# Performance work log

Hardware: AMD Instinct MI355X
Metric: run time of the kernel (lower is better)

Reference implementation:

```python
import jax, jax.numpy as jnp
import numpy as np

N_NODES = 10000
N_EDGES = 160000
C = 64        # latent channels
H = 512       # MLP hidden width
L = 2         # allegro layers
NB = 8        # bessel basis size
CUT = 2.0     # radial cutoff
AVG = 3.0     # avg_num_neighbors


def setup_inputs() -> dict:
    key = jax.random.key(0)
    ks = jax.random.split(key, 12)
    positions = jax.random.normal(ks[0], (N_NODES, 3), jnp.float32)
    species = jax.random.randint(ks[1], (N_NODES,), 0, 2, jnp.int32)
    senders = jax.random.randint(ks[2], (N_EDGES,), 0, N_NODES, jnp.int32)
    receivers = jax.random.randint(ks[3], (N_EDGES,), 0, N_NODES, jnp.int32)
    w = lambda k, shape, fan: (jax.random.normal(k, shape, jnp.float32) / np.sqrt(fan).astype(np.float32))
    return dict(
        positions=positions,
        W_emb1=w(ks[4], (NB + 4, H), NB + 4),
        W_emb2=w(ks[5], (H, C), H),
        W_v=w(ks[6], (C, C), C),
        W_env=w(ks[7], (L, C, C), C),
        W_lat1=w(ks[8], (L, 3 * C, H), 3 * C),
        W_lat2=w(ks[9], (L, H, C), H),
        W_mix=w(ks[10], (L, C, 2 * C), C),
        W_out=w(ks[11], (C,), C),
        species=species, senders=senders, receivers=receivers,
    )


def reference(positions, W_emb1, W_emb2, W_v, W_env, W_lat1, W_lat2, W_mix, W_out,
              species, senders, receivers):
    node_attrs = jax.nn.one_hot(species, 2, dtype=positions.dtype)   # [N,2]
    r = positions[receivers] - positions[senders]                    # [E,3] edge vectors ('1o')
    d = jnp.sqrt(jnp.sum(r * r, axis=-1))                            # [E]
    dsafe = jnp.maximum(d, 1e-6)
    u = r / dsafe[:, None]                                           # unit vectors = l=1 spherical harmonics

    # radial basis: Bessel functions with smooth polynomial cutoff envelope
    xc = d / CUT
    env = jnp.where(xc < 1.0, (1.0 - xc ** 2) ** 2, 0.0)             # [E]
    nvec = jnp.arange(1, NB + 1, dtype=positions.dtype)
    bessel = jnp.sqrt(2.0 / CUT) * jnp.sin(nvec * jnp.pi * xc[:, None]) / dsafe[:, None]
    rad = bessel * env[:, None]                                      # [E,NB]

    # two-body latent embedding
    feat = jnp.concatenate([rad, node_attrs[senders], node_attrs[receivers]], axis=-1)  # [E,NB+4]
    x = (jax.nn.silu(feat @ W_emb1) @ W_emb2) * env[:, None]         # [E,C]
    # initial equivariant edge features (C channels of 1o)
    V = (x @ W_v)[:, :, None] * u[:, None, :]                        # [E,C,3]

    inv_sqrt2 = 1.0 / jnp.sqrt(2.0)
    for l in range(L):
        # environment density: scatter edge basis to sender nodes, gather back per edge
        w_e = x @ W_env[l]                                           # [E,C]
        rho1 = jax.ops.segment_sum(w_e[:, :, None] * u[:, None, :], senders,
                                   num_segments=N_NODES) / AVG       # [N,C,3] (1o density)
        rho0 = jax.ops.segment_sum(w_e, senders, num_segments=N_NODES) / AVG  # [N,C] (0e density)
        rho1_e = rho1[senders]                                       # [E,C,3]
        rho0_e = rho0[senders]                                       # [E,C]

        # channel-wise Clebsch-Gordan tensor products (lmax=1 paths)
        tp_scal = jnp.einsum('eci,eci->ec', V, rho1_e)               # 1o x 1o -> 0e
        tp_vec1 = V * rho0_e[:, :, None]                             # 1o x 0e -> 1o
        tp_vec2 = jnp.cross(V, rho1_e)                               # 1o x 1o -> 1e

        # latent update (residual, envelope-gated)
        lat_in = jnp.concatenate([x, tp_scal, rho0_e], axis=-1)      # [E,3C]
        dx = (jax.nn.silu(lat_in @ W_lat1[l]) @ W_lat2[l]) * env[:, None]
        x = (x + dx) * inv_sqrt2

        # equivariant update: latent-conditioned mix of tensor-product outputs
        mix = x @ W_mix[l]                                           # [E,2C]
        V = mix[:, :C, None] * tp_vec1 + mix[:, C:, None] * tp_vec2  # [E,C,3]

    # per-edge scalar readout, scatter-reduced to nodes
    e_edge = (x @ W_out) * env                                       # [E]
    node_energy = jax.ops.segment_sum(e_edge, receivers, num_segments=N_NODES) / AVG
    return node_energy
```

## Files before the change

### kernel.cpp

```cpp
#include <hip/hip_runtime.h>
#include <hip/hip_bf16.h>

#define E_NUM 160000
#define NN 10000
#define PI_F 3.14159265358979323846f

using u16 = unsigned short;
using u32 = unsigned int;
typedef short bf16x8 __attribute__((ext_vector_type(8)));
typedef float f32x4 __attribute__((ext_vector_type(4)));
typedef u32 u32x4 __attribute__((ext_vector_type(4)));

__device__ __forceinline__ float silu_fast(float z) {
    return z * __builtin_amdgcn_rcpf(1.0f + __expf(-z));
}
__device__ __forceinline__ float bfb2f(u32 bits16) {
    return __builtin_bit_cast(float, bits16 << 16);
}
__device__ __forceinline__ u32 f2bfb(float f) {
    return (u32)__builtin_bit_cast(u16, __float2bfloat16(f));
}
__device__ __forceinline__ u32 pack2(float lo, float hi) {
    return f2bfb(lo) | (f2bfb(hi) << 16);
}

__global__ void k_detect(const u16* __restrict__ posraw, int* __restrict__ flag) {
    int i = blockIdx.x * 256 + threadIdx.x;
    if (i >= 15000) return;
    float v = bfb2f((u32)posraw[2 * i]);
    if (!(fabsf(v) < 1e4f)) atomicOr(flag, 1);
}

__global__ void k_cvt_all(const void* s0, const void* s1, const void* s2,
                          const void* s3, const void* s4, const void* s5,
                          const void* s6, const void* s7, const void* s8,
                          float* __restrict__ dst, const int* __restrict__ flag) {
    int i = blockIdx.x * 256 + threadIdx.x;
    if (i >= 359792) return;
    const void* src; int off;
    if      (i < 30000)  { src = s0; off = i; }
    else if (i < 36144)  { src = s1; off = i - 30000; }
    else if (i < 68912)  { src = s2; off = i - 36144; }
    else if (i < 73008)  { src = s3; off = i - 68912; }
    else if (i < 81200)  { src = s4; off = i - 73008; }
    else if (i < 277808) { src = s5; off = i - 81200; }
    else if (i < 343344) { src = s6; off = i - 277808; }
    else if (i < 359728) { src = s7; off = i - 343344; }
    else                 { src = s8; off = i - 359728; }
    if (*flag) dst[i] = ((const float*)src)[off];
    else       dst[i] = bfb2f((u32)((const u16*)src)[off]);
}

__global__ void k_pack(const float* __restrict__ W, int K, int Nshift,
                       u16* __restrict__ pk) {
    int i = blockIdx.x * 256 + threadIdx.x;
    int total = K << Nshift;
    if (i >= total) return;
    int k = i >> Nshift, n = i & ((1 << Nshift) - 1);
    float w = W[i];
    u16 h = (u16)f2bfb(w);
    float r = w - bfb2f((u32)h);
    int idx = ((((k >> 3) << Nshift) + n) << 4) + (k & 7);
    pk[idx] = h; pk[idx + 8] = (u16)f2bfb(r);
}

__global__ void k_pack_emb1(const float* __restrict__ W , u16* __restrict__ pk) {
    int i = blockIdx.x * 256 + threadIdx.x;
    if (i >= 64 * 512) return;
    int k = i >> 9, n = i & 511;
    u16 out = 0;
    if (k < 24) {
        out = (u16)f2bfb(W[(k % 12) * 512 + n]);
    } else if (k < 36) {
        float w = W[(k - 24) * 512 + n];
        u16 h = (u16)f2bfb(w);
        out = (u16)f2bfb(w - bfb2f((u32)h));
    }
    pk[((((k >> 3) << 9) + n) << 4) + (k & 7)] = out;
}

__global__ void k_hist(const int* __restrict__ senders, int* __restrict__ counts) {
    int e = blockIdx.x * 256 + threadIdx.x;
    if (e < E_NUM) atomicAdd(&counts[senders[e]], 1);
}

__global__ __launch_bounds__(1024) void k_scan(const int* __restrict__ counts,
                                               int* __restrict__ rowstart) {
    __shared__ int part[1024];
    int t = threadIdx.x;
    int base = t * 10;
    int local[10];
    int sum = 0;
    #pragma unroll
    for (int i = 0; i < 10; i++) {
        int v = (base + i < NN) ? counts[base + i] : 0;
        local[i] = sum; sum += v;
    }
    part[t] = sum;
    __syncthreads();
    for (int off = 1; off < 1024; off <<= 1) {
        int v = (t >= off) ? part[t - off] : 0;
        __syncthreads();
        part[t] += v;
        __syncthreads();
    }
    int pre = (t == 0) ? 0 : part[t - 1];
    #pragma unroll
    for (int i = 0; i < 10; i++)
        if (base + i < NN) rowstart[base + i] = pre + local[i];
    if (t == 1023) rowstart[NN] = part[1023];
}

__global__ void k_copy_int(const int* __restrict__ src, int* __restrict__ dst, int n) {
    int i = blockIdx.x * 256 + threadIdx.x;
    if (i < n) dst[i] = src[i];
}

__global__ void k_fill(const int* __restrict__ senders, int* __restrict__ cursor,
                       int* __restrict__ edge_list) {
    int e = blockIdx.x * 256 + threadIdx.x;
    if (e >= E_NUM) return;
    int pos = atomicAdd(&cursor[senders[e]], 1);
    edge_list[pos] = e;
}

__global__ void k_geom(const float* __restrict__ posf, const int* __restrict__ species,
                       const int* __restrict__ senders, const int* __restrict__ receivers,
                       const int* __restrict__ edge_list,
                       int* __restrict__ ssend, int* __restrict__ srecv,
                       float* __restrict__ ux, float* __restrict__ uy, float* __restrict__ uz,
                       float* __restrict__ envb, u32* __restrict__ latin) {
    int e = blockIdx.x * 256 + threadIdx.x;
    if (e >= E_NUM) return;
    int orig = edge_list[e];
    int s = senders[orig], r = receivers[orig];
    ssend[e] = s; srecv[e] = r;
    float rx = posf[3 * r + 0] - posf[3 * s + 0];
    float ry = posf[3 * r + 1] - posf[3 * s + 1];
    float rz = posf[3 * r + 2] - posf[3 * s + 2];
    float d = sqrtf(rx * rx + ry * ry + rz * rz);
    float inv = 1.0f / fmaxf(d, 1e-6f);
    ux[e] = rx * inv; uy[e] = ry * inv; uz[e] = rz * inv;
    float xc = d * 0.5f;
    float env = 0.0f;
    if (xc < 1.0f) { float t = 1.0f - xc * xc; env = t * t; }
    envb[e] = env;
    float ft[12];
    float se = env * inv;
    #pragma unroll
    for (int n = 1; n <= 8; n++) ft[n - 1] = __sinf((float)n * PI_F * xc) * se;
    int ss = species[s], sr = species[r];
    ft[8] = (ss == 0) ? 1.0f : 0.0f;
    ft[9] = (ss == 1) ? 1.0f : 0.0f;
    ft[10] = (sr == 0) ? 1.0f : 0.0f;
    ft[11] = (sr == 1) ? 1.0f : 0.0f;
    u32 ch[32];
    #pragma unroll
    for (int i = 0; i < 32; i++) ch[i] = 0;
    #pragma unroll
    for (int j = 0; j < 6; j++) {
        u32 hp = f2bfb(ft[2 * j]) | (f2bfb(ft[2 * j + 1]) << 16);
        float l0 = ft[2 * j] - bfb2f(f2bfb(ft[2 * j]));
        float l1 = ft[2 * j + 1] - bfb2f(f2bfb(ft[2 * j + 1]));
        ch[j] = hp;
        ch[12 + j] = hp;
        ch[6 + j] = pack2(l0, l1);
    }
    #pragma unroll
    for (int g = 0; g < 8; g++) {
        u32x4 v = {ch[4 * g], ch[4 * g + 1], ch[4 * g + 2], ch[4 * g + 3]};
        *(u32x4*)(latin + (((size_t)g * E_NUM + e) << 2)) = v;
    }
}

__global__ __launch_bounds__(256) void k_rho_gather(
    const float* __restrict__ we, const int* __restrict__ rowstart,
    const float* __restrict__ ux, const float* __restrict__ uy,
    const float* __restrict__ uz,
    float* __restrict__ rho0, float* __restrict__ rho1) {
    int wv = (blockIdx.x * 256 + threadIdx.x) >> 6;
    int c = threadIdx.x & 63;
    if (wv >= NN) return;
    int start = rowstart[wv], end = rowstart[wv + 1];
    float s0 = 0.0f, sx = 0.0f, sy = 0.0f, sz = 0.0f;
    for (int j = start; j < end; j++) {
        float w = we[(size_t)j * 64 + c];
        float a = ux[j], b = uy[j], g = uz[j];
        s0 += w;
        sx = fmaf(w, a, sx);
        sy = fmaf(w, b, sy);
        sz = fmaf(w, g, sz);
    }
    const float inv3 = 1.0f / 3.0f;
    rho0[(size_t)wv * 64 + c] = s0 * inv3;
    rho1[(size_t)wv * 192 + 3 * c + 0] = sx * inv3;
    rho1[(size_t)wv * 192 + 3 * c + 1] = sy * inv3;
    rho1[(size_t)wv * 192 + 3 * c + 2] = sz * inv3;
}

template<int KSTEPS, int MODE, int HASLO, int FUSEWE, int STAGE>
__global__ __launch_bounds__(512, 4) void k_mlp(
    const u32* __restrict__ latin,
    const u16* __restrict__ W1pk, const u16* __restrict__ W2pk,
    const float* __restrict__ envb,
    u32* __restrict__ xout,
    const u16* __restrict__ wepk,
    float* __restrict__ webuf,
    const u32* __restrict__ xin,
    const u32* __restrict__ x0t,
    const int* __restrict__ ssend,
    const float* __restrict__ ux, const float* __restrict__ uy,
    const float* __restrict__ uz,
    const float* __restrict__ rho0A, const float* __restrict__ rho1A,
    const float* __restrict__ rho0B, const float* __restrict__ rho1B,
    const u16* __restrict__ wvpk, const u16* __restrict__ wmpk,
    const float* __restrict__ WoutP, const int* __restrict__ srecv,
    float* __restrict__ node_acc) {
    constexpr int ROWDW = KSTEPS * 16;
    constexpr int INAREG = KSTEPS * 4096;
    constexpr int SMEMSZ = INAREG + ((STAGE == 2) ? (2 * 16640) : 32768);
    __shared__ __align__(16) char smem[SMEMSZ];
    u32* inA = (u32*)smem;
    u16* hA  = (u16*)(smem + INAREG);
    float* tbA = (float*)(smem + INAREG);
    u16* mb   = (u16*)(smem + INAREG + 16640);
    u32* mb32 = (u32*)(smem + INAREG + 16640);
    u32* xt0  = (u32*)(smem + INAREG + 16640);
    int lane = threadIdx.x & 63;
    int sub = threadIdx.x >> 6;
    int w = __builtin_amdgcn_readfirstlane(sub);
    int l15 = lane & 15, quad = lane >> 4;
    int e0 = blockIdx.x * 64;
    int e = e0 + lane;

    if (STAGE == 0) {
        constexpr int CPW = (KSTEPS * 4) / 8;
        #pragma unroll
        for (int j = 0; j < CPW; j++) {
            int c = w * CPW + j;
            u32x4 v = *(const u32x4*)(latin + (((size_t)c * E_NUM + e) << 2));
            int slot = (c & ~7) | ((c ^ lane) & 7);
            *(u32x4*)(&inA[lane * ROWDW + slot * 4]) = v;
        }
        __syncthreads();
    } else {
        {
            int c = w;
            u32x4 v = *(const u32x4*)(xin + (((size_t)c * E_NUM + e) << 2));
            int slot = (c & ~7) | ((c ^ lane) & 7);
            *(u32x4*)(&inA[lane * ROWDW + slot * 4]) = v;
        }
        if (STAGE == 2) {
            u32x4 v = *(const u32x4*)(x0t + (((size_t)w * E_NUM + e) << 2));
            int slot = (w ^ lane) & 7;
            *(u32x4*)(&xt0[lane * 32 + slot * 4]) = v;
        }
        __syncthreads();
        int mt = w & 3;
        int ntbA = (w >> 2) * 2;
        f32x4 accA[2];
        accA[0] = (f32x4){0.f, 0.f, 0.f, 0.f};
        accA[1] = (f32x4){0.f, 0.f, 0.f, 0.f};
        #pragma unroll
        for (int ks = 0; ks < 2; ks++) {
            int c = ks * 4 + quad;
            int m = mt * 16 + l15;
            bf16x8 af;
            if (STAGE == 1) {
                int slot = (c & ~7) | ((c ^ m) & 7);
                af = *(const bf16x8*)(&inA[m * ROWDW + slot * 4]);
            } else {
                int slot = (c ^ m) & 7;
                af = *(const bf16x8*)(&xt0[m * 32 + slot * 4]);
            }
            #pragma unroll
            for (int nti = 0; nti < 2; nti++) {
                int n = (ntbA + nti) * 16 + l15;
                const u16* bp = wvpk + ((((size_t)c << 6) + n) << 4);
                bf16x8 bh = *(const bf16x8*)(bp);
                accA[nti] = __builtin_amdgcn_mfma_f32_16x16x32_bf16(af, bh, accA[nti], 0, 0, 0);
                bf16x8 bl = *(const bf16x8*)(bp + 8);
                accA[nti] = __builtin_amdgcn_mfma_f32_16x16x32_bf16(af, bl, accA[nti], 0, 0, 0);
            }
        }
        f32x4 accM[4];
        if (STAGE == 2) {
            #pragma unroll
            for (int i = 0; i < 4; i++) accM[i] = (f32x4){0.f, 0.f, 0.f, 0.f};
            int nbM = (w >> 2) * 4;
            #pragma unroll
            for (int ks = 0; ks < 2; ks++) {
                int c = ks * 4 + quad;
                int m = mt * 16 + l15;
                int slot = (c & ~7) | ((c ^ m) & 7);
                bf16x8 af = *(const bf16x8*)(&inA[m * ROWDW + slot * 4]);
                #pragma unroll
                for (int nti = 0; nti < 4; nti++) {
                    int n = (nbM + nti) * 16 + l15;
                    const u16* bp = wmpk + ((((size_t)c << 7) + n) << 4);
                    bf16x8 bh = *(const bf16x8*)(bp);
                    accM[nti] = __builtin_amdgcn_mfma_f32_16x16x32_bf16(af, bh, accM[nti], 0, 0, 0);
                    bf16x8 bl = *(const bf16x8*)(bp + 8);
                    accM[nti] = __builtin_amdgcn_mfma_f32_16x16x32_bf16(af, bl, accM[nti], 0, 0, 0);
                }
            }
        }
        __syncthreads();
        #pragma unroll
        for (int nti = 0; nti < 2; nti++) {
            #pragma unroll
            for (int r = 0; r < 4; r++) {
                int rowD = mt * 16 + quad * 4 + r;
                int colD = (ntbA + nti) * 16 + l15;
                tbA[colD * 65 + rowD] = accA[nti][r];
            }
        }
        if (STAGE == 2) {
            int sel = (w >= 4) ? 1 : 0;
            #pragma unroll
            for (int nti = 0; nti < 4; nti++) {
                #pragma unroll
                for (int r = 0; r < 4; r++) {
                    int rowD = mt * 16 + quad * 4 + r;
                    int colD = nti * 16 + l15;
                    mb[((colD * 65 + rowD) << 1) + sel] = (u16)f2bfb(accM[nti][r]);
                }
            }
        }
        __syncthreads();
        int c0 = w * 8;
        float av[8], m1v[8], m2v[8];
        #pragma unroll
        for (int i = 0; i < 8; i++) av[i] = tbA[(c0 + i) * 65 + lane];
        if (STAGE == 2) {
            #pragma unroll
            for (int i = 0; i < 8; i++) {
                u32 pv = mb32[(c0 + i) * 65 + lane];
                m1v[i] = bfb2f(pv & 0xffffu);
                m2v[i] = bfb2f(pv >> 16);
            }
        }
        int s = ssend[e];
        float u0 = ux[e], u1 = uy[e], u2 = uz[e];
        float ts[8], rr[8];
        if (STAGE == 1) {
            const float* r1 = rho1A + (size_t)s * 192;
            const float* r0 = rho0A + (size_t)s * 64;
            #pragma unroll
            for (int i = 0; i < 8; i++) {
                int c = c0 + i;
                float dot = u0 * r1[3 * c] + u1 * r1[3 * c + 1] + u2 * r1[3 * c + 2];
                ts[i] = av[i] * dot;
                rr[i] = r0[c];
            }
        } else {
            const float* r1A = rho1A + (size_t)s * 192;
            const float* r0A = rho0A + (size_t)s * 64;
            const float* r1B = rho1B + (size_t)s * 192;
            const float* r0B = rho0B + (size_t)s * 64;
            #pragma unroll
            for (int i = 0; i < 8; i++) {
                int c = c0 + i;
                float v0 = av[i] * u0, v1 = av[i] * u1, v2 = av[i] * u2;
                float aA0 = r1A[3 * c], aA1 = r1A[3 * c + 1], aA2 = r1A[3 * c + 2];
                float rc = r0A[c];
                float w0 = m1v[i] * v0 * rc + m2v[i] * (v1 * aA2 - v2 * aA1);
                float w1 = m1v[i] * v1 * rc + m2v[i] * (v2 * aA0 - v0 * aA2);
                float w2 = m1v[i] * v2 * rc + m2v[i] * (v0 * aA1 - v1 * aA0);
                ts[i] = w0 * r1B[3 * c] + w1 * r1B[3 * c + 1] + w2 * r1B[3 * c + 2];
                rr[i] = r0B[c];
            }
        }
        u32x4 tv, rv;
        #pragma unroll
        for (int j = 0; j < 4; j++) {
            tv[j] = pack2(ts[2 * j], ts[2 * j + 1]);
            rv[j] = pack2(rr[2 * j], rr[2 * j + 1]);
        }
        {
            int c = 8 + w;
            int slot = (c & ~7) | ((c ^ lane) & 7);
            *(u32x4*)(&inA[lane * ROWDW + slot * 4]) = tv;
        }
        {
            int c = 16 + w;
            int slot = (c & ~7) | ((c ^ lane) & 7);
            *(u32x4*)(&inA[lane * ROWDW + slot * 4]) = rv;
        }
        __syncthreads();
    }

    f32x4 acc2[2];
    acc2[0] = (f32x4){0.f, 0.f, 0.f, 0.f};
    acc2[1] = (f32x4){0.f, 0.f, 0.f, 0.f};
    int nt2 = w & 3;
    int mt2a = (w >> 2) * 2;
    int p = 0;

    #pragma unroll
    for (int it = 0; it < 5; it++) {
        f32x4 acc[4];
        if (it < 4) {
            #pragma unroll
            for (int mt = 0; mt < 4; mt++) acc[mt] = (f32x4){0.f, 0.f, 0.f, 0.f};
            __builtin_amdgcn_s_setprio(1);
            #pragma unroll
            for (int ks = 0; ks < KSTEPS; ks++) {
                int c = ks * 4 + quad;
                bf16x8 afr[4];
                #pragma unroll
                for (int mt = 0; mt < 4; mt++) {
                    int m = mt * 16 + l15;
                    int slot = (c & ~7) | ((c ^ m) & 7);
                    afr[mt] = *(const bf16x8*)(&inA[m * ROWDW + slot * 4]);
                }
                int n = it * 128 + w * 16 + l15;
                const u16* bp = W1pk + ((((size_t)c << 9) + n) << 4);
                bf16x8 bh = *(const bf16x8*)(bp);
                #pragma unroll
                for (int mt = 0; mt < 4; mt++)
                    acc[mt] = __builtin_amdgcn_mfma_f32_16x16x32_bf16(afr[mt], bh, acc[mt], 0, 0, 0);
                if (HASLO) {
                    bf16x8 bl = *(const bf16x8*)(bp + 8);
                    #pragma unroll
                    for (int mt = 0; mt < 4; mt++)
                        acc[mt] = __builtin_amdgcn_mfma_f32_16x16x32_bf16(afr[mt], bl, acc[mt], 0, 0, 0);
                }
            }
            __builtin_amdgcn_s_setprio(0);
        }
        if (it > 0) {
            const u16* hAr = hA + (p ^ 1) * 8192;
            __builtin_amdgcn_s_setprio(1);
            #pragma unroll
            for (int ks = 0; ks < 4; ks++) {
                int c = ks * 4 + quad;
                int m0 = mt2a * 16 + l15;
                int m1i = m0 + 16;
                int s0 = (c & 8) | ((c ^ m0) & 7);
                int s1 = (c & 8) | ((c ^ m1i) & 7);
                bf16x8 a0 = *(const bf16x8*)(&hAr[m0 * 128 + s0 * 8]);
                bf16x8 a1 = *(const bf16x8*)(&hAr[m1i * 128 + s1 * 8]);
                const u16* bp = W2pk + ((((size_t)((it - 1) * 16 + c) << 6) + nt2 * 16 + l15) << 4);
                bf16x8 bh = *(const bf16x8*)(bp);
                acc2[0] = __builtin_amdgcn_mfma_f32_16x16x32_bf16(a0, bh, acc2[0], 0, 0, 0);
                acc2[1] = __builtin_amdgcn_mfma_f32_16x16x32_bf16(a1, bh, acc2[1], 0, 0, 0);
                bf16x8 bl = *(const bf16x8*)(bp + 8);
                acc2[0] = __builtin_amdgcn_mfma_f32_16x16x32_bf16(a0, bl, acc2[0], 0, 0, 0);
                acc2[1] = __builtin_amdgcn_mfma_f32_16x16x32_bf16(a1, bl, acc2[1], 0, 0, 0);
            }
            __builtin_amdgcn_s_setprio(0);
        }
        if (it < 4) {
            u16* hAw = hA + p * 8192;
            int kh = w * 16 + l15;
            int c = kh >> 3;
            #pragma unroll
            for (int mt = 0; mt < 4; mt++) {
                #pragma unroll
                for (int r = 0; r < 4; r++) {
                    int m = mt * 16 + quad * 4 + r;
                    float s = silu_fast(acc[mt][r]);
                    int slot = (c & 8) | ((c ^ m) & 7);
                    hAw[m * 128 + slot * 8 + (kh & 7)] = (u16)f2bfb(s);
                }
            }
            __syncthreads();
        }
        p ^= 1;
    }
    float xo[8];
    if (MODE) {
        int c = w;
        int slot = (c & ~7) | ((c ^ lane) & 7);
        #pragma unroll
        for (int i = 0; i < 4; i++) {
            u32 pv = inA[lane * ROWDW + slot * 4 + i];
            xo[2 * i]     = bfb2f(pv & 0xffffu);
            xo[2 * i + 1] = bfb2f(pv >> 16);
        }
    }
    __syncthreads();
    float* epi = (float*)inA;
    #pragma unroll
    for (int mi = 0; mi < 2; mi++) {
        #pragma unroll
        for (int r = 0; r < 4; r++) {
            int m = (mt2a + mi) * 16 + quad * 4 + r;
            int c = nt2 * 16 + l15;
            epi[c * 65 + m] = acc2[mi][r];
        }
    }
    __syncthreads();
    float env = envb[e];
    const float is2 = 0.70710678118654752f;
    float resv[8];
    #pragma unroll
    for (int i = 0; i < 8; i++) {
        int c = w * 8 + i;
        float v = epi[c * 65 + lane];
        float res;
        if (MODE) res = (xo[i] + v * env) * is2;
        else      res = v * env;
        resv[i] = res;
        if (FUSEWE) epi[c * 65 + lane] = res;
    }
    if (STAGE != 2) {
        u32x4 tv;
        #pragma unroll
        for (int j = 0; j < 4; j++) tv[j] = pack2(resv[2 * j], resv[2 * j + 1]);
        *(u32x4*)(xout + (((size_t)w * E_NUM + e) << 2)) = tv;
    }
    if (STAGE == 2) {
        float* red = (float*)(smem + 20480);
        float pd = 0.0f;
        #pragma unroll
        for (int i = 0; i < 8; i++) pd = fmaf(resv[i], WoutP[w * 8 + i], pd);
        red[w * 64 + lane] = pd;
        __syncthreads();
        if (w == 0) {
            float sum = 0.0f;
            #pragma unroll
            for (int ww = 0; ww < 8; ww++) sum += red[ww * 64 + lane];
            atomicAdd(&node_acc[srecv[e]], sum * env * (1.0f / 3.0f));
        }
    }
    if (FUSEWE) {
        __syncthreads();
        int mt = w & 3;
        int ntb = (w >> 2) * 2;
        f32x4 accw[2];
        accw[0] = (f32x4){0.f, 0.f, 0.f, 0.f};
        accw[1] = (f32x4){0.f, 0.f, 0.f, 0.f};
        #pragma unroll
        for (int ks = 0; ks < 2; ks++) {
            bf16x8 af;
            #pragma unroll
            for (int j = 0; j < 8; j++)
                af[j] = (short)f2bfb(epi[(ks * 32 + quad * 8 + j) * 65 + mt * 16 + l15]);
            #pragma unroll
            for (int nti = 0; nti < 2; nti++) {
                int n4 = (ntb + nti) * 16 + l15;
                const u16* bp = wepk + ((((size_t)(ks * 4 + quad) << 6) + n4) << 4);
                bf16x8 bh = *(const bf16x8*)(bp);
                accw[nti] = __builtin_amdgcn_mfma_f32_16x16x32_bf16(af, bh, accw[nti], 0, 0, 0);
                bf16x8 bl = *(const bf16x8*)(bp + 8);
                accw[nti] = __builtin_amdgcn_mfma_f32_16x16x32_bf16(af, bl, accw[nti], 0, 0, 0);
            }
        }
        #pragma unroll
        for (int nti = 0; nti < 2; nti++) {
            #pragma unroll
            for (int r = 0; r < 4; r++) {
                int rowD = mt * 16 + quad * 4 + r;
                int colD = (ntb + nti) * 16 + l15;
                webuf[(size_t)(e0 + rowD) * 64 + colD] = accw[nti][r];
            }
        }
    }
}

__global__ void k_out(const float* __restrict__ node_acc, void* __restrict__ out,
                      const int* __restrict__ flag) {
    int n = blockIdx.x * 256 + threadIdx.x;
    if (n >= NN) return;
    float v = node_acc[n];
    if (*flag) ((float*)out)[n] = v;
    else       ((u16*)out)[n] = (u16)f2bfb(v);
}

extern "C" void kernel_launch(void* const* d_in, const int* in_sizes, int n_in,
                              void* d_out, int out_size, void* d_ws, size_t ws_size,
                              hipStream_t stream) {
    const void* posr   = d_in[0];
    const void* Wemb1r = d_in[1];
    const void* Wemb2r = d_in[2];
    const void* Wvr    = d_in[3];
    const void* Wenvr  = d_in[4];
    const void* Wlat1r = d_in[5];
    const void* Wlat2r = d_in[6];
    const void* Wmixr  = d_in[7];
    const void* Woutr  = d_in[8];
    const int* species   = (const int*)d_in[9];
    const int* senders   = (const int*)d_in[10];
    const int* receivers = (const int*)d_in[11];

    char* p = (char*)d_ws;
    auto alloc = [&](size_t bytes) -> void* {
        void* rp = (void*)p;
        p += (bytes + 255) & ~(size_t)255;
        return rp;
    };
    int*   flag  = (int*)alloc(4);
    float* wbuf  = (float*)alloc(359792 * 4);
    float* posf  = wbuf;
    float* Wemb1 = wbuf + 30000;
    float* Wemb2 = wbuf + 36144;
    float* Wv    = wbuf + 68912;
    float* Wenv  = wbuf + 73008;
    float* Wlat1 = wbuf + 81200;
    float* Wlat2 = wbuf + 277808;
    float* Wmix  = wbuf + 343344;
    float* Wout  = wbuf + 359728;
    const size_t E = E_NUM;
    float* ux   = (float*)alloc(E * 4);
    float* uy   = (float*)alloc(E * 4);
    float* uz   = (float*)alloc(E * 4);
    float* envb = (float*)alloc(E * 4);
    float* rho0A = (float*)alloc((size_t)NN * 64 * 4);
    float* rho1A = (float*)alloc((size_t)NN * 192 * 4);
    float* rho0B = (float*)alloc((size_t)NN * 64 * 4);
    float* rho1B = (float*)alloc((size_t)NN * 192 * 4);
    float* node_acc = (float*)alloc((size_t)NN * 4);
    int* counts    = (int*)alloc((size_t)NN * 4);
    int* rowstart  = (int*)alloc((size_t)(NN + 1) * 4);
    int* cursor    = (int*)alloc((size_t)NN * 4);
    int* edge_list = (int*)alloc(E * 4);
    int* ssend     = (int*)alloc(E * 4);
    int* srecv     = (int*)alloc(E * 4);
    void* unionbuf = alloc(96 * E * 4);
    u32*   latin = (u32*)unionbuf;
    float* webuf = (float*)unionbuf + (size_t)32 * E;
    u32* x0 = (u32*)alloc(32 * E * 4);
    u32* x1 = (u32*)alloc(32 * E * 4);
    u16* w1pk = (u16*)alloc(2 * 196608 * 2);
    u16* w2pk = (u16*)alloc(2 * 65536 * 2);
    u16* e1pk = (u16*)alloc(65536 * 2);
    u16* e2pk = (u16*)alloc(65536 * 2);
    u16* we0pk = (u16*)alloc(8192 * 2);
    u16* we1pk = (u16*)alloc(8192 * 2);
    u16* wvpk  = (u16*)alloc(8192 * 2);
    u16* wmpk  = (u16*)alloc(16384 * 2);

    hipMemsetAsync(flag, 0, 4, stream);
    hipMemsetAsync(counts, 0, (size_t)NN * 4, stream);
    hipMemsetAsync(node_acc, 0, (size_t)NN * 4, stream);

    k_detect<<<(15000 + 255) / 256, 256, 0, stream>>>((const u16*)posr, flag);

    k_cvt_all<<<(359792 + 255) / 256, 256, 0, stream>>>(
        posr, Wemb1r, Wemb2r, Wvr, Wenvr, Wlat1r, Wlat2r, Wmixr, Woutr,
        wbuf, flag);

    k_pack_emb1<<<128, 256, 0, stream>>>(Wemb1, e1pk);
    k_pack<<<128, 256, 0, stream>>>(Wemb2, 512, 6, e2pk);
    k_pack<<<16, 256, 0, stream>>>(Wenv, 64, 6, we0pk);
    k_pack<<<16, 256, 0, stream>>>(Wenv + 4096, 64, 6, we1pk);
    k_pack<<<16, 256, 0, stream>>>(Wv, 64, 6, wvpk);
    k_pack<<<32, 256, 0, stream>>>(Wmix, 64, 7, wmpk);
    for (int l = 0; l < 2; l++) {
        k_pack<<<384, 256, 0, stream>>>(Wlat1 + l * 98304, 192, 9,
                                        w1pk + l * 196608);
        k_pack<<<128, 256, 0, stream>>>(Wlat2 + l * 32768, 512, 6,
                                        w2pk + l * 65536);
    }

    k_hist<<<625, 256, 0, stream>>>(senders, counts);
    k_scan<<<1, 1024, 0, stream>>>(counts, rowstart);
    k_copy_int<<<(NN + 255) / 256, 256, 0, stream>>>(rowstart, cursor, NN);
    k_fill<<<625, 256, 0, stream>>>(senders, cursor, edge_list);

    k_geom<<<625, 256, 0, stream>>>(posf, species, senders, receivers, edge_list,
                                    ssend, srecv, ux, uy, uz, envb, latin);
    k_mlp<2, 0, 0, 1, 0><<<2500, 512, 0, stream>>>(
        latin, e1pk, e2pk, envb, x0, we0pk, webuf,
        nullptr, nullptr, nullptr, nullptr, nullptr, nullptr,
        nullptr, nullptr, nullptr, nullptr, nullptr, nullptr,
        nullptr, nullptr, nullptr);

    k_rho_gather<<<2500, 256, 0, stream>>>(webuf, rowstart, ux, uy, uz,
                                           rho0A, rho1A);
    k_mlp<6, 1, 1, 1, 1><<<2500, 512, 0, stream>>>(
        nullptr, w1pk, w2pk, envb, x1, we1pk, webuf,
        x0, nullptr, ssend, ux, uy, uz, rho0A, rho1A, nullptr, nullptr,
        wvpk, nullptr, nullptr, nullptr, nullptr);

    k_rho_gather<<<2500, 256, 0, stream>>>(webuf, rowstart, ux, uy, uz,
                                           rho0B, rho1B);
    k_mlp<6, 1, 1, 0, 2><<<2500, 512, 0, stream>>>(
        nullptr, w1pk + 196608, w2pk + 65536, envb, nullptr, nullptr, nullptr,
        x1, x0, ssend, ux, uy, uz, rho0A, rho1A, rho0B, rho1B,
        wvpk, wmpk, Wout, srecv, node_acc);

    k_out<<<(NN + 255) / 256, 256, 0, stream>>>(node_acc, d_out, flag);
}
```

Measured before the change: 433.2 us.

## Merge preprocessing kernels and trim zero-padded embedding input writes

Merges the dtype conversion with the sender histogram, and the edge-list fill with all weight packing kernels, into two combined launches. The scan now writes the cursor array directly, which removes a copy kernel. k_geom writes only the 5 non-zero chunks of the embedding input, and the stage-0 MLP load zero-fills the rest instead of reading it from memory. The rho gather loop is also unrolled by two. This cuts roughly 13 kernel launches and some global traffic, at the cost of branchier combined kernels.

```diff
diff --git a/kernel.cpp b/kernel.cpp
--- a/kernel.cpp
+++ b/kernel.cpp
@@ -31,29 +31,35 @@
     if (!(fabsf(v) < 1e4f)) atomicOr(flag, 1);
 }
 
-__global__ void k_cvt_all(const void* s0, const void* s1, const void* s2,
-                          const void* s3, const void* s4, const void* s5,
-                          const void* s6, const void* s7, const void* s8,
-                          float* __restrict__ dst, const int* __restrict__ flag) {
-    int i = blockIdx.x * 256 + threadIdx.x;
-    if (i >= 359792) return;
-    const void* src; int off;
-    if      (i < 30000)  { src = s0; off = i; }
-    else if (i < 36144)  { src = s1; off = i - 30000; }
-    else if (i < 68912)  { src = s2; off = i - 36144; }
-    else if (i < 73008)  { src = s3; off = i - 68912; }
-    else if (i < 81200)  { src = s4; off = i - 73008; }
-    else if (i < 277808) { src = s5; off = i - 81200; }
-    else if (i < 343344) { src = s6; off = i - 277808; }
-    else if (i < 359728) { src = s7; off = i - 343344; }
-    else                 { src = s8; off = i - 359728; }
-    if (*flag) dst[i] = ((const float*)src)[off];
-    else       dst[i] = bfb2f((u32)((const u16*)src)[off]);
-}
-
-__global__ void k_pack(const float* __restrict__ W, int K, int Nshift,
-                       u16* __restrict__ pk) {
-    int i = blockIdx.x * 256 + threadIdx.x;
+__global__ void k_prep1(const void* s0, const void* s1, const void* s2,
+                        const void* s3, const void* s4, const void* s5,
+                        const void* s6, const void* s7, const void* s8,
+                        float* __restrict__ dst, const int* __restrict__ flag,
+                        const int* __restrict__ senders, int* __restrict__ counts) {
+    int bid = blockIdx.x;
+    if (bid < 1406) {
+        int i = bid * 256 + threadIdx.x;
+        if (i >= 359792) return;
+        const void* src; int off;
+        if      (i < 30000)  { src = s0; off = i; }
+        else if (i < 36144)  { src = s1; off = i - 30000; }
+        else if (i < 68912)  { src = s2; off = i - 36144; }
+        else if (i < 73008)  { src = s3; off = i - 68912; }
+        else if (i < 81200)  { src = s4; off = i - 73008; }
+        else if (i < 277808) { src = s5; off = i - 81200; }
+        else if (i < 343344) { src = s6; off = i - 277808; }
+        else if (i < 359728) { src = s7; off = i - 343344; }
+        else                 { src = s8; off = i - 359728; }
+        if (*flag) dst[i] = ((const float*)src)[off];
+        else       dst[i] = bfb2f((u32)((const u16*)src)[off]);
+    } else {
+        int e = (bid - 1406) * 256 + threadIdx.x;
+        if (e < E_NUM) atomicAdd(&counts[senders[e]], 1);
+    }
+}
+
+__device__ __forceinline__ void pack_body(const float* __restrict__ W, int K, int Nshift,
+                                          u16* __restrict__ pk, int i) {
     int total = K << Nshift;
     if (i >= total) return;
     int k = i >> Nshift, n = i & ((1 << Nshift) - 1);
@@ -64,8 +70,8 @@
     pk[idx] = h; pk[idx + 8] = (u16)f2bfb(r);
 }
 
-__global__ void k_pack_emb1(const float* __restrict__ W , u16* __restrict__ pk) {
-    int i = blockIdx.x * 256 + threadIdx.x;
+__device__ __forceinline__ void pack_emb1_body(const float* __restrict__ W ,
+                                               u16* __restrict__ pk, int i) {
     if (i >= 64 * 512) return;
     int k = i >> 9, n = i & 511;
     u16 out = 0;
@@ -79,13 +85,41 @@
     pk[((((k >> 3) << 9) + n) << 4) + (k & 7)] = out;
 }
 
-__global__ void k_hist(const int* __restrict__ senders, int* __restrict__ counts) {
-    int e = blockIdx.x * 256 + threadIdx.x;
-    if (e < E_NUM) atomicAdd(&counts[senders[e]], 1);
+__global__ void k_prep2(const int* __restrict__ senders, int* __restrict__ cursor,
+                        int* __restrict__ edge_list,
+                        const float* __restrict__ Wemb1, const float* __restrict__ Wemb2,
+                        const float* __restrict__ Wenv, const float* __restrict__ Wv,
+                        const float* __restrict__ Wmix, const float* __restrict__ Wlat1,
+                        const float* __restrict__ Wlat2,
+                        u16* __restrict__ e1pk, u16* __restrict__ e2pk,
+                        u16* __restrict__ we0pk, u16* __restrict__ we1pk,
+                        u16* __restrict__ wvpk, u16* __restrict__ wmpk,
+                        u16* __restrict__ w1pk, u16* __restrict__ w2pk) {
+    int bid = blockIdx.x;
+    int t = threadIdx.x;
+    if (bid < 625) {
+        int e = bid * 256 + t;
+        if (e >= E_NUM) return;
+        int pos = atomicAdd(&cursor[senders[e]], 1);
+        edge_list[pos] = e;
+        return;
+    }
+    bid -= 625;
+    if      (bid < 128)  pack_emb1_body(Wemb1, e1pk, bid * 256 + t);
+    else if (bid < 256)  pack_body(Wemb2, 512, 6, e2pk, (bid - 128) * 256 + t);
+    else if (bid < 272)  pack_body(Wenv, 64, 6, we0pk, (bid - 256) * 256 + t);
+    else if (bid < 288)  pack_body(Wenv + 4096, 64, 6, we1pk, (bid - 272) * 256 + t);
+    else if (bid < 304)  pack_body(Wv, 64, 6, wvpk, (bid - 288) * 256 + t);
+    else if (bid < 336)  pack_body(Wmix, 64, 7, wmpk, (bid - 304) * 256 + t);
+    else if (bid < 720)  pack_body(Wlat1, 192, 9, w1pk, (bid - 336) * 256 + t);
+    else if (bid < 1104) pack_body(Wlat1 + 98304, 192, 9, w1pk + 196608, (bid - 720) * 256 + t);
+    else if (bid < 1232) pack_body(Wlat2, 512, 6, w2pk, (bid - 1104) * 256 + t);
+    else                 pack_body(Wlat2 + 32768, 512, 6, w2pk + 65536, (bid - 1232) * 256 + t);
 }
 
 __global__ __launch_bounds__(1024) void k_scan(const int* __restrict__ counts,
-                                               int* __restrict__ rowstart) {
+                                               int* __restrict__ rowstart,
+                                               int* __restrict__ cursor) {
     __shared__ int part[1024];
     int t = threadIdx.x;
     int base = t * 10;
@@ -107,21 +141,12 @@
     int pre = (t == 0) ? 0 : part[t - 1];
     #pragma unroll
     for (int i = 0; i < 10; i++)
-        if (base + i < NN) rowstart[base + i] = pre + local[i];
+        if (base + i < NN) {
+            int v = pre + local[i];
+            rowstart[base + i] = v;
+            cursor[base + i] = v;
+        }
     if (t == 1023) rowstart[NN] = part[1023];
-}
-
-__global__ void k_copy_int(const int* __restrict__ src, int* __restrict__ dst, int n) {
-    int i = blockIdx.x * 256 + threadIdx.x;
-    if (i < n) dst[i] = src[i];
-}
-
-__global__ void k_fill(const int* __restrict__ senders, int* __restrict__ cursor,
-                       int* __restrict__ edge_list) {
-    int e = blockIdx.x * 256 + threadIdx.x;
-    if (e >= E_NUM) return;
-    int pos = atomicAdd(&cursor[senders[e]], 1);
-    edge_list[pos] = e;
 }
 
 __global__ void k_geom(const float* __restrict__ posf, const int* __restrict__ species,
@@ -154,9 +179,9 @@
     ft[9] = (ss == 1) ? 1.0f : 0.0f;
     ft[10] = (sr == 0) ? 1.0f : 0.0f;
     ft[11] = (sr == 1) ? 1.0f : 0.0f;
-    u32 ch[32];
-    #pragma unroll
-    for (int i = 0; i < 32; i++) ch[i] = 0;
+    u32 ch[20];
+    #pragma unroll
+    for (int i = 0; i < 20; i++) ch[i] = 0;
     #pragma unroll
     for (int j = 0; j < 6; j++) {
         u32 hp = f2bfb(ft[2 * j]) | (f2bfb(ft[2 * j + 1]) << 16);
@@ -167,7 +192,7 @@
         ch[6 + j] = pack2(l0, l1);
     }
     #pragma unroll
-    for (int g = 0; g < 8; g++) {
+    for (int g = 0; g < 5; g++) {
         u32x4 v = {ch[4 * g], ch[4 * g + 1], ch[4 * g + 2], ch[4 * g + 3]};
         *(u32x4*)(latin + (((size_t)g * E_NUM + e) << 2)) = v;
     }
@@ -183,13 +208,28 @@
     if (wv >= NN) return;
     int start = rowstart[wv], end = rowstart[wv + 1];
     float s0 = 0.0f, sx = 0.0f, sy = 0.0f, sz = 0.0f;
-    for (int j = start; j < end; j++) {
-        float w = we[(size_t)j * 64 + c];
-        float a = ux[j], b = uy[j], g = uz[j];
-        s0 += w;
-        sx = fmaf(w, a, sx);
-        sy = fmaf(w, b, sy);
-        sz = fmaf(w, g, sz);
+    int j = start;
+    for (; j + 2 <= end; j += 2) {
+        float w0 = we[(size_t)j * 64 + c];
+        float w1 = we[(size_t)(j + 1) * 64 + c];
+        float a0 = ux[j], b0 = uy[j], g0 = uz[j];
+        float a1 = ux[j + 1], b1 = uy[j + 1], g1 = uz[j + 1];
+        s0 += w0;
+        sx = fmaf(w0, a0, sx);
+        sy = fmaf(w0, b0, sy);
+        sz = fmaf(w0, g0, sz);
+        s0 += w1;
+        sx = fmaf(w1, a1, sx);
+        sy = fmaf(w1, b1, sy);
+        sz = fmaf(w1, g1, sz);
+    }
+    if (j < end) {
+        float w0 = we[(size_t)j * 64 + c];
+        float a0 = ux[j], b0 = uy[j], g0 = uz[j];
+        s0 += w0;
+        sx = fmaf(w0, a0, sx);
+        sy = fmaf(w0, b0, sy);
+        sz = fmaf(w0, g0, sz);
     }
     const float inv3 = 1.0f / 3.0f;
     rho0[(size_t)wv * 64 + c] = s0 * inv3;
@@ -234,14 +274,10 @@
     int e = e0 + lane;
 
     if (STAGE == 0) {
-        constexpr int CPW = (KSTEPS * 4) / 8;
-        #pragma unroll
-        for (int j = 0; j < CPW; j++) {
-            int c = w * CPW + j;
-            u32x4 v = *(const u32x4*)(latin + (((size_t)c * E_NUM + e) << 2));
-            int slot = (c & ~7) | ((c ^ lane) & 7);
-            *(u32x4*)(&inA[lane * ROWDW + slot * 4]) = v;
-        }
+        u32x4 v = (u32x4){0, 0, 0, 0};
+        if (w < 5) v = *(const u32x4*)(latin + (((size_t)w * E_NUM + e) << 2));
+        int slot = (w ^ lane) & 7;
+        *(u32x4*)(&inA[lane * ROWDW + slot * 4]) = v;
         __syncthreads();
     } else {
         {
@@ -638,27 +674,16 @@
 
     k_detect<<<(15000 + 255) / 256, 256, 0, stream>>>((const u16*)posr, flag);
 
-    k_cvt_all<<<(359792 + 255) / 256, 256, 0, stream>>>(
+    k_prep1<<<2031, 256, 0, stream>>>(
         posr, Wemb1r, Wemb2r, Wvr, Wenvr, Wlat1r, Wlat2r, Wmixr, Woutr,
-        wbuf, flag);
-
-    k_pack_emb1<<<128, 256, 0, stream>>>(Wemb1, e1pk);
-    k_pack<<<128, 256, 0, stream>>>(Wemb2, 512, 6, e2pk);
-    k_pack<<<16, 256, 0, stream>>>(Wenv, 64, 6, we0pk);
-    k_pack<<<16, 256, 0, stream>>>(Wenv + 4096, 64, 6, we1pk);
-    k_pack<<<16, 256, 0, stream>>>(Wv, 64, 6, wvpk);
-    k_pack<<<32, 256, 0, stream>>>(Wmix, 64, 7, wmpk);
-    for (int l = 0; l < 2; l++) {
-        k_pack<<<384, 256, 0, stream>>>(Wlat1 + l * 98304, 192, 9,
-                                        w1pk + l * 196608);
-        k_pack<<<128, 256, 0, stream>>>(Wlat2 + l * 32768, 512, 6,
-                                        w2pk + l * 65536);
-    }
-
-    k_hist<<<625, 256, 0, stream>>>(senders, counts);
-    k_scan<<<1, 1024, 0, stream>>>(counts, rowstart);
-    k_copy_int<<<(NN + 255) / 256, 256, 0, stream>>>(rowstart, cursor, NN);
-    k_fill<<<625, 256, 0, stream>>>(senders, cursor, edge_list);
+        wbuf, flag, senders, counts);
+
+    k_scan<<<1, 1024, 0, stream>>>(counts, rowstart, cursor);
+
+    k_prep2<<<1985, 256, 0, stream>>>(
+        senders, cursor, edge_list,
+        Wemb1, Wemb2, Wenv, Wv, Wmix, Wlat1, Wlat2,
+        e1pk, e2pk, we0pk, we1pk, wvpk, wmpk, w1pk, w2pk);
 
     k_geom<<<625, 256, 0, stream>>>(posf, species, senders, receivers, edge_list,
                                     ssend, srecv, ux, uy, uz, envb, latin);
```

New measurement: 412.6 us. 4.8% less time.
